# Kernel optimization log

Hardware: AMD Instinct MI355X
Metric: run time of the kernel (lower is better)

The kernel has to match this reference:

```python
import jax, jax.numpy as jnp
import numpy as np

N_NODES = 50000
N_EDGES = 800000
D_IN = 64      # entity_embedding_size_in
D_REL = 64     # relation_embedding_size
D_OUT = 64     # entity_embedding_size_out
IN_DIM = 2 * D_IN + D_REL  # 192


def mish(x):
    return x * jnp.tanh(jax.nn.softplus(x))


def setup_inputs() -> dict:
    key = jax.random.key(0)
    k1, k2, k3, k4 = jax.random.split(key, 4)
    triple_features = jax.random.normal(k1, (N_EDGES, IN_DIM), dtype=jnp.float32)
    # row 0: destination node; row 1: unique slot id per edge (guarantees no
    # duplicate sparse indices, so torch's coalesce would be a no-op)
    dst = jax.random.randint(k2, (N_EDGES,), 0, N_NODES)
    slot = jnp.arange(N_EDGES)
    indices = jnp.stack([dst, slot], axis=0).astype(jnp.int64)
    # Kaiming-uniform-ish init for the two linear layers (bias=False)
    bound1 = float(np.sqrt(6.0 / IN_DIM))
    W_triple = jax.random.uniform(k3, (D_OUT, IN_DIM), minval=-bound1, maxval=bound1, dtype=jnp.float32)
    bound2 = float(np.sqrt(6.0 / D_OUT))
    w_att = jax.random.uniform(k4, (1, D_OUT), minval=-bound2, maxval=bound2, dtype=jnp.float32)
    return {
        "triple_features": triple_features,
        "sparse_triple_adjacency_list_indices": indices,
        "W_triple": W_triple,
        "w_att": w_att,
    }


def reference(triple_features, sparse_triple_adjacency_list_indices, W_triple, w_att):
    # dropout is identity in eval mode
    h = triple_features @ W_triple.T                      # [E, D_OUT]
    a = mish(h @ w_att[0])                                # [E]
    dst = sparse_triple_adjacency_list_indices[0]         # [E] destination node
    # segment softmax of attention logits grouped by destination node
    seg_max = jax.ops.segment_max(a, dst, num_segments=N_NODES)  # [N]
    seg_max = jnp.where(jnp.isfinite(seg_max), seg_max, 0.0)
    e = jnp.exp(a - seg_max[dst])                         # [E]
    denom = jax.ops.segment_sum(e, dst, num_segments=N_NODES)    # [N]
    p = e / denom[dst]                                    # [E]
    # attention-weighted scatter-sum aggregation per node
    out = jax.ops.segment_sum(h * p[:, None], dst, num_segments=N_NODES)  # [N, D_OUT]
    return out
```

## Files before the change

kernel.cpp:

```cpp
#include <hip/hip_runtime.h>
#include <hip/hip_bf16.h>
#include <math.h>


typedef __bf16  bf16x8 __attribute__((ext_vector_type(8)));
typedef float   f32x4  __attribute__((ext_vector_type(4)));

#define KDIM 192
#define LDSS 200

__device__ inline unsigned short f2bf(float f) {
    unsigned u = __float_as_uint(f);
    unsigned r = u + 0x7fffu + ((u >> 16) & 1u);
    return (unsigned short)(r >> 16);
}
__device__ inline float bf2f(unsigned short h) {
    return __uint_as_float(((unsigned)h) << 16);
}

__global__ void init_kernel(int* __restrict__ count, int* __restrict__ cursor, int n_nodes,
                            const float* __restrict__ W, unsigned short* __restrict__ wbf, int wn) {
    int i = blockIdx.x * blockDim.x + threadIdx.x;
    int stride = gridDim.x * blockDim.x;
    for (int j = i; j < n_nodes; j += stride) { count[j] = 0; cursor[j] = 0; }
    for (int j = i; j < wn; j += stride) wbf[j] = f2bf(W[j]);
}

__global__ __launch_bounds__(256)
void gemm_att_kernel(const float* __restrict__ X, const unsigned short* __restrict__ wbf,
                     const float* __restrict__ w_att, const int* __restrict__ dst,
                     unsigned short* __restrict__ h_bf, float* __restrict__ a_out,
                     int* __restrict__ count, int E) {
    __shared__ unsigned short lds_x[64 * LDSS];
    const int e0  = blockIdx.x * 64;
    const int tid = threadIdx.x;

    const float4* Xv = (const float4*)(X + (size_t)e0 * KDIM);
    #pragma unroll
    for (int it = 0; it < 12; ++it) {
        int f = it * 256 + tid;
        int e = f / 48;
        int c = f - e * 48;
        float4 v;
        if (e0 + e < E) v = Xv[f];
        else            v = make_float4(0.f, 0.f, 0.f, 0.f);
        unsigned short* p = &lds_x[e * LDSS + c * 4];
        p[0] = f2bf(v.x); p[1] = f2bf(v.y); p[2] = f2bf(v.z); p[3] = f2bf(v.w);
    }
    __syncthreads();

    const int wave  = tid >> 6;
    const int lane  = tid & 63;
    const int n16   = lane & 15;
    const int quad  = lane >> 4;
    const int m0    = wave * 16;

    f32x4 acc[4] = {{0,0,0,0},{0,0,0,0},{0,0,0,0},{0,0,0,0}};
    #pragma unroll
    for (int kk = 0; kk < 6; ++kk) {
        bf16x8 afrag = *(const bf16x8*)&lds_x[(m0 + n16) * LDSS + kk * 32 + quad * 8];
        #pragma unroll
        for (int nt = 0; nt < 4; ++nt) {
            bf16x8 bfrag = *(const bf16x8*)&wbf[(nt * 16 + n16) * KDIM + kk * 32 + quad * 8];
            acc[nt] = __builtin_amdgcn_mfma_f32_16x16x32_bf16(afrag, bfrag, acc[nt], 0, 0, 0);
        }
    }

    float wa[4];
    #pragma unroll
    for (int nt = 0; nt < 4; ++nt) wa[nt] = w_att[nt * 16 + n16];

    float pa[4] = {0.f, 0.f, 0.f, 0.f};
    #pragma unroll
    for (int nt = 0; nt < 4; ++nt) {
        #pragma unroll
        for (int r = 0; r < 4; ++r) {
            int e = e0 + m0 + quad * 4 + r;
            float v = acc[nt][r];
            if (e < E) h_bf[(size_t)e * 64 + nt * 16 + n16] = f2bf(v);
            pa[r] += v * wa[nt];
        }
    }
    #pragma unroll
    for (int r = 0; r < 4; ++r) {
        float s = pa[r];
        s += __shfl_xor(s, 1);
        s += __shfl_xor(s, 2);
        s += __shfl_xor(s, 4);
        s += __shfl_xor(s, 8);
        pa[r] = s;
    }
    if (n16 == 0) {
        #pragma unroll
        for (int r = 0; r < 4; ++r) {
            int e = e0 + m0 + quad * 4 + r;
            if (e >= E) continue;
            float x = pa[r];
            float mv;
            if (x > 15.0f) {
                mv = x;
            } else {
                float ex = expf(x);
                float t  = (1.0f + ex);
                t = t * t;
                mv = x * (t - 1.0f) / (t + 1.0f);
            }
            a_out[e] = mv;
            atomicAdd(&count[dst[e]], 1);
        }
    }
}

__global__ __launch_bounds__(256)
void scan1_kernel(const int* __restrict__ count, int* __restrict__ offsets,
                  int* __restrict__ bsum, int n) {
    __shared__ int tmp[256];
    int i = blockIdx.x * 256 + threadIdx.x;
    int v = (i < n) ? count[i] : 0;
    tmp[threadIdx.x] = v;
    __syncthreads();
    #pragma unroll
    for (int off = 1; off < 256; off <<= 1) {
        int t = (threadIdx.x >= off) ? tmp[threadIdx.x - off] : 0;
        __syncthreads();
        tmp[threadIdx.x] += t;
        __syncthreads();
    }
    if (i < n) offsets[i] = tmp[threadIdx.x] - v;
    if (threadIdx.x == 255) bsum[blockIdx.x] = tmp[255];
}

__global__ __launch_bounds__(256)
void scan2_kernel(int* __restrict__ bsum, int nb) {
    __shared__ int tmp[256];
    int v = (threadIdx.x < nb) ? bsum[threadIdx.x] : 0;
    tmp[threadIdx.x] = v;
    __syncthreads();
    #pragma unroll
    for (int off = 1; off < 256; off <<= 1) {
        int t = (threadIdx.x >= off) ? tmp[threadIdx.x - off] : 0;
        __syncthreads();
        tmp[threadIdx.x] += t;
        __syncthreads();
    }
    if (threadIdx.x < nb) bsum[threadIdx.x] = tmp[threadIdx.x] - v;
}

__global__ __launch_bounds__(256)
void scan3_kernel(int* __restrict__ offsets, const int* __restrict__ bsum, int n, int E) {
    int i = blockIdx.x * 256 + threadIdx.x;
    if (i < n) offsets[i] += bsum[blockIdx.x];
    if (i == 0) offsets[n] = E;
}

__global__ __launch_bounds__(256)
void scatter_kernel(const int* __restrict__ dst, const int* __restrict__ offsets,
                    int* __restrict__ cursor, int* __restrict__ perm, int E) {
    int e = blockIdx.x * 256 + threadIdx.x;
    if (e < E) {
        int d = dst[e];
        int pos = offsets[d] + atomicAdd(&cursor[d], 1);
        perm[pos] = e;
    }
}

__global__ __launch_bounds__(256)
void aggregate_kernel(const unsigned short* __restrict__ h_bf, const float* __restrict__ a,
                      const int* __restrict__ perm, const int* __restrict__ offsets,
                      float* __restrict__ out, int N) {
    int node = (int)((blockIdx.x * (unsigned)blockDim.x + threadIdx.x) >> 6);
    int lane = threadIdx.x & 63;
    if (node >= N) return;
    int start = offsets[node];
    int end   = offsets[node + 1];
    if (start == end) { out[(size_t)node * 64 + lane] = 0.0f; return; }

    float m = -INFINITY;
    for (int i = start + lane; i < end; i += 64) m = fmaxf(m, a[perm[i]]);
    #pragma unroll
    for (int s = 32; s >= 1; s >>= 1) m = fmaxf(m, __shfl_xor(m, s));

    float acc = 0.0f, ssum = 0.0f;
    for (int i = start; i < end; ++i) {
        int e = perm[i];
        float w = __expf(a[e] - m);
        ssum += w;
        acc  += w * bf2f(h_bf[(size_t)e * 64 + lane]);
    }
    out[(size_t)node * 64 + lane] = acc / ssum;
}

extern "C" void kernel_launch(void* const* d_in, const int* in_sizes, int n_in,
                              void* d_out, int out_size, void* d_ws, size_t ws_size,
                              hipStream_t stream) {
    const float* X     = (const float*)d_in[0];
    const int*   idx   = (const int*)d_in[1];
    const float* W     = (const float*)d_in[2];
    const float* w_att = (const float*)d_in[3];

    const int E       = in_sizes[1] / 2;
    const int n_nodes = out_size / 64;
    const int wn      = in_sizes[2];
    const int* dst    = idx;

    char* ws = (char*)d_ws;
    unsigned short* wbf  = (unsigned short*)ws;
    unsigned short* h_bf = (unsigned short*)(ws + 24576);
    size_t off = 24576 + (size_t)E * 64 * 2;
    float* a       = (float*)(ws + off);  off += (size_t)E * 4;
    int*   perm    = (int*)(ws + off);    off += (size_t)E * 4;
    int*   count   = (int*)(ws + off);    off += (size_t)n_nodes * 4;
    int*   cursor  = (int*)(ws + off);    off += (size_t)n_nodes * 4;
    int*   offsets = (int*)(ws + off);    off += (size_t)(n_nodes + 1) * 4;
    int*   bsum    = (int*)(ws + off);

    float* out = (float*)d_out;

    init_kernel<<<256, 256, 0, stream>>>(count, cursor, n_nodes, W, wbf, wn);

    int nblk_gemm = (E + 63) / 64;
    gemm_att_kernel<<<nblk_gemm, 256, 0, stream>>>(X, wbf, w_att, dst, h_bf, a, count, E);

    int nb = (n_nodes + 255) / 256;
    scan1_kernel<<<nb, 256, 0, stream>>>(count, offsets, bsum, n_nodes);
    scan2_kernel<<<1, 256, 0, stream>>>(bsum, nb);
    scan3_kernel<<<nb, 256, 0, stream>>>(offsets, bsum, n_nodes, E);

    scatter_kernel<<<(E + 255) / 256, 256, 0, stream>>>(dst, offsets, cursor, perm, E);

    int nblk_agg = (n_nodes + 3) / 4;
    aggregate_kernel<<<nblk_agg, 256, 0, stream>>>(h_bf, a, perm, offsets, out, n_nodes);
}
```

Baseline: 1.063 ms.

## Fuse softmax aggregation into GEMM via atomic scatter, drop CSR build

Removes the CSR construction (count, scan, scatter) and the separate aggregate kernel. The GEMM kernel now computes exp(mish(logit)) per edge and atomically adds the weighted h rows into the zeroed output and the per-node denominators. A small normalization kernel then divides each row by its denominator. The segment-max subtraction is dropped, so this depends on logits staying small enough for exp not to overflow, and the per-node sums are now built from many float atomics in nondeterministic order.

```diff
diff --git a/kernel.cpp b/kernel.cpp
--- a/kernel.cpp
+++ b/kernel.cpp
@@ -14,23 +14,22 @@
     unsigned r = u + 0x7fffu + ((u >> 16) & 1u);
     return (unsigned short)(r >> 16);
 }
-__device__ inline float bf2f(unsigned short h) {
-    return __uint_as_float(((unsigned)h) << 16);
-}
 
-__global__ void init_kernel(int* __restrict__ count, int* __restrict__ cursor, int n_nodes,
+__global__ void init_kernel(float* __restrict__ out, float* __restrict__ denom, int n_nodes,
                             const float* __restrict__ W, unsigned short* __restrict__ wbf, int wn) {
     int i = blockIdx.x * blockDim.x + threadIdx.x;
     int stride = gridDim.x * blockDim.x;
-    for (int j = i; j < n_nodes; j += stride) { count[j] = 0; cursor[j] = 0; }
+    float4* o4 = (float4*)out;
+    int n4 = n_nodes * 16;
+    for (int j = i; j < n4; j += stride) o4[j] = make_float4(0.f, 0.f, 0.f, 0.f);
+    for (int j = i; j < n_nodes; j += stride) denom[j] = 0.f;
     for (int j = i; j < wn; j += stride) wbf[j] = f2bf(W[j]);
 }
 
 __global__ __launch_bounds__(256)
 void gemm_att_kernel(const float* __restrict__ X, const unsigned short* __restrict__ wbf,
                      const float* __restrict__ w_att, const int* __restrict__ dst,
-                     unsigned short* __restrict__ h_bf, float* __restrict__ a_out,
-                     int* __restrict__ count, int E) {
+                     float* __restrict__ out, float* __restrict__ denom, int E) {
     __shared__ unsigned short lds_x[64 * LDSS];
     const int e0  = blockIdx.x * 64;
     const int tid = threadIdx.x;
@@ -44,8 +43,9 @@
         float4 v;
         if (e0 + e < E) v = Xv[f];
         else            v = make_float4(0.f, 0.f, 0.f, 0.f);
-        unsigned short* p = &lds_x[e * LDSS + c * 4];
-        p[0] = f2bf(v.x); p[1] = f2bf(v.y); p[2] = f2bf(v.z); p[3] = f2bf(v.w);
+        unsigned px = ((unsigned)f2bf(v.y) << 16) | (unsigned)f2bf(v.x);
+        unsigned py = ((unsigned)f2bf(v.w) << 16) | (unsigned)f2bf(v.z);
+        *(uint2*)&lds_x[e * LDSS + c * 4] = make_uint2(px, py);
     }
     __syncthreads();
 
@@ -74,12 +74,7 @@
     #pragma unroll
     for (int nt = 0; nt < 4; ++nt) {
         #pragma unroll
-        for (int r = 0; r < 4; ++r) {
-            int e = e0 + m0 + quad * 4 + r;
-            float v = acc[nt][r];
-            if (e < E) h_bf[(size_t)e * 64 + nt * 16 + n16] = f2bf(v);
-            pa[r] += v * wa[nt];
-        }
+        for (int r = 0; r < 4; ++r) pa[r] += acc[nt][r] * wa[nt];
     }
     #pragma unroll
     for (int r = 0; r < 4; ++r) {
@@ -90,104 +85,55 @@
         s += __shfl_xor(s, 8);
         pa[r] = s;
     }
-    if (n16 == 0) {
+
+    const int rsel = n16 & 3;
+    float x = (rsel == 0) ? pa[0] : (rsel == 1) ? pa[1] : (rsel == 2) ? pa[2] : pa[3];
+    int  e_r = e0 + m0 + quad * 4 + rsel;
+    float w = 0.f;
+    int   d = 0;
+    if (e_r < E) {
+        d = dst[e_r];
+        float mv;
+        if (x > 15.0f) {
+            mv = x;
+        } else {
+            float ex = expf(x);
+            float t  = (1.0f + ex);
+            t = t * t;
+            mv = x * (t - 1.0f) / (t + 1.0f);
+        }
+        w = __expf(mv);
+    }
+    if (n16 < 4 && e_r < E) atomicAdd(&denom[d], w);
+
+    const int base = lane & 0x30;
+    float wr[4];
+    int   dr[4];
+    wr[0] = __shfl(w, base | 0); dr[0] = __shfl(d, base | 0);
+    wr[1] = __shfl(w, base | 1); dr[1] = __shfl(d, base | 1);
+    wr[2] = __shfl(w, base | 2); dr[2] = __shfl(d, base | 2);
+    wr[3] = __shfl(w, base | 3); dr[3] = __shfl(d, base | 3);
+
+    #pragma unroll
+    for (int nt = 0; nt < 4; ++nt) {
         #pragma unroll
         for (int r = 0; r < 4; ++r) {
-            int e = e0 + m0 + quad * 4 + r;
-            if (e >= E) continue;
-            float x = pa[r];
-            float mv;
-            if (x > 15.0f) {
-                mv = x;
-            } else {
-                float ex = expf(x);
-                float t  = (1.0f + ex);
-                t = t * t;
-                mv = x * (t - 1.0f) / (t + 1.0f);
-            }
-            a_out[e] = mv;
-            atomicAdd(&count[dst[e]], 1);
+            if (wr[r] > 0.f)
+                atomicAdd(&out[(size_t)dr[r] * 64 + nt * 16 + n16], wr[r] * acc[nt][r]);
         }
     }
 }
 
 __global__ __launch_bounds__(256)
-void scan1_kernel(const int* __restrict__ count, int* __restrict__ offsets,
-                  int* __restrict__ bsum, int n) {
-    __shared__ int tmp[256];
+void norm_kernel(float* __restrict__ out, const float* __restrict__ denom, int n_nodes) {
     int i = blockIdx.x * 256 + threadIdx.x;
-    int v = (i < n) ? count[i] : 0;
-    tmp[threadIdx.x] = v;
-    __syncthreads();
-    #pragma unroll
-    for (int off = 1; off < 256; off <<= 1) {
-        int t = (threadIdx.x >= off) ? tmp[threadIdx.x - off] : 0;
-        __syncthreads();
-        tmp[threadIdx.x] += t;
-        __syncthreads();
-    }
-    if (i < n) offsets[i] = tmp[threadIdx.x] - v;
-    if (threadIdx.x == 255) bsum[blockIdx.x] = tmp[255];
-}
-
-__global__ __launch_bounds__(256)
-void scan2_kernel(int* __restrict__ bsum, int nb) {
-    __shared__ int tmp[256];
-    int v = (threadIdx.x < nb) ? bsum[threadIdx.x] : 0;
-    tmp[threadIdx.x] = v;
-    __syncthreads();
-    #pragma unroll
-    for (int off = 1; off < 256; off <<= 1) {
-        int t = (threadIdx.x >= off) ? tmp[threadIdx.x - off] : 0;
-        __syncthreads();
-        tmp[threadIdx.x] += t;
-        __syncthreads();
-    }
-    if (threadIdx.x < nb) bsum[threadIdx.x] = tmp[threadIdx.x] - v;
-}
-
-__global__ __launch_bounds__(256)
-void scan3_kernel(int* __restrict__ offsets, const int* __restrict__ bsum, int n, int E) {
-    int i = blockIdx.x * 256 + threadIdx.x;
-    if (i < n) offsets[i] += bsum[blockIdx.x];
-    if (i == 0) offsets[n] = E;
-}
-
-__global__ __launch_bounds__(256)
-void scatter_kernel(const int* __restrict__ dst, const int* __restrict__ offsets,
-                    int* __restrict__ cursor, int* __restrict__ perm, int E) {
-    int e = blockIdx.x * 256 + threadIdx.x;
-    if (e < E) {
-        int d = dst[e];
-        int pos = offsets[d] + atomicAdd(&cursor[d], 1);
-        perm[pos] = e;
-    }
-}
-
-__global__ __launch_bounds__(256)
-void aggregate_kernel(const unsigned short* __restrict__ h_bf, const float* __restrict__ a,
-                      const int* __restrict__ perm, const int* __restrict__ offsets,
-                      float* __restrict__ out, int N) {
-    int node = (int)((blockIdx.x * (unsigned)blockDim.x + threadIdx.x) >> 6);
-    int lane = threadIdx.x & 63;
-    if (node >= N) return;
-    int start = offsets[node];
-    int end   = offsets[node + 1];
-    if (start == end) { out[(size_t)node * 64 + lane] = 0.0f; return; }
-
-    float m = -INFINITY;
-    for (int i = start + lane; i < end; i += 64) m = fmaxf(m, a[perm[i]]);
-    #pragma unroll
-    for (int s = 32; s >= 1; s >>= 1) m = fmaxf(m, __shfl_xor(m, s));
-
-    float acc = 0.0f, ssum = 0.0f;
-    for (int i = start; i < end; ++i) {
-        int e = perm[i];
-        float w = __expf(a[e] - m);
-        ssum += w;
-        acc  += w * bf2f(h_bf[(size_t)e * 64 + lane]);
-    }
-    out[(size_t)node * 64 + lane] = acc / ssum;
+    int n4 = n_nodes * 16;
+    if (i >= n4) return;
+    float dnm = denom[i >> 4];
+    float r = (dnm > 0.f) ? 1.0f / dnm : 0.0f;
+    float4 v = ((float4*)out)[i];
+    v.x *= r; v.y *= r; v.z *= r; v.w *= r;
+    ((float4*)out)[i] = v;
 }
 
 extern "C" void kernel_launch(void* const* d_in, const int* in_sizes, int n_in,
@@ -204,30 +150,16 @@
     const int* dst    = idx;
 
     char* ws = (char*)d_ws;
-    unsigned short* wbf  = (unsigned short*)ws;
-    unsigned short* h_bf = (unsigned short*)(ws + 24576);
-    size_t off = 24576 + (size_t)E * 64 * 2;
-    float* a       = (float*)(ws + off);  off += (size_t)E * 4;
-    int*   perm    = (int*)(ws + off);    off += (size_t)E * 4;
-    int*   count   = (int*)(ws + off);    off += (size_t)n_nodes * 4;
-    int*   cursor  = (int*)(ws + off);    off += (size_t)n_nodes * 4;
-    int*   offsets = (int*)(ws + off);    off += (size_t)(n_nodes + 1) * 4;
-    int*   bsum    = (int*)(ws + off);
+    unsigned short* wbf   = (unsigned short*)ws;
+    float*          denom = (float*)(ws + 24576);
 
     float* out = (float*)d_out;
 
-    init_kernel<<<256, 256, 0, stream>>>(count, cursor, n_nodes, W, wbf, wn);
+    init_kernel<<<256, 256, 0, stream>>>(out, denom, n_nodes, W, wbf, wn);
 
     int nblk_gemm = (E + 63) / 64;
-    gemm_att_kernel<<<nblk_gemm, 256, 0, stream>>>(X, wbf, w_att, dst, h_bf, a, count, E);
+    gemm_att_kernel<<<nblk_gemm, 256, 0, stream>>>(X, wbf, w_att, dst, out, denom, E);
 
-    int nb = (n_nodes + 255) / 256;
-    scan1_kernel<<<nb, 256, 0, stream>>>(count, offsets, bsum, n_nodes);
-    scan2_kernel<<<1, 256, 0, stream>>>(bsum, nb);
-    scan3_kernel<<<nb, 256, 0, stream>>>(offsets, bsum, n_nodes, E);
-
-    scatter_kernel<<<(E + 255) / 256, 256, 0, stream>>>(dst, offsets, cursor, perm, E);
-
-    int nblk_agg = (n_nodes + 3) / 4;
-    aggregate_kernel<<<nblk_agg, 256, 0, stream>>>(h_bf, a, perm, offsets, out, n_nodes);
+    int nblk_norm = (n_nodes * 16 + 255) / 256;
+    norm_kernel<<<nblk_norm, 256, 0, stream>>>(out, denom, n_nodes);
 }
```

After: 896.6 us. 15.7% less time.
